# Kernel tuning notes

Hardware: AMD Instinct MI355X
Metric: run time of the kernel (lower is better)

Reference implementation:

```python
import jax, jax.numpy as jnp
import numpy as np

B, S, D = 2, 2048, 2048
H = 16
Q_LORA, KV_LORA = 1536, 512
D_NOPE, D_ROPE = 128, 64
D_QK = D_NOPE + D_ROPE  # 192
D_V = 128
EPS = 1e-6
SCALE = D_QK ** -0.5


def rms_norm(x, w):
    var = jnp.mean(jnp.square(x), axis=-1, keepdims=True)
    return x * jax.lax.rsqrt(var + EPS) * w


def apply_rotary_emb(x, freqs_cis):
    # x: [B, S, h, dr]; freqs_cis: [S, dr//2, 2] (cos, sin); interleaved pairs
    b, s, h, dr = x.shape
    xp = x.reshape(b, s, h, dr // 2, 2)
    x0, x1 = xp[..., 0], xp[..., 1]
    cos = freqs_cis[None, :, None, :, 0]
    sin = freqs_cis[None, :, None, :, 1]
    o0 = x0 * cos - x1 * sin
    o1 = x0 * sin + x1 * cos
    return jnp.stack([o0, o1], axis=-1).reshape(b, s, h, dr)


def setup_inputs() -> dict:
    key = jax.random.key(0)
    ks = jax.random.split(key, 8)
    std = 0.02
    x = jax.random.normal(ks[0], (B, S, D), jnp.float32)
    inv_freq = 1.0 / (10000.0 ** (np.arange(0, D_ROPE, 2, dtype=np.float32) / D_ROPE))
    ang = np.outer(np.arange(S, dtype=np.float32), inv_freq)  # [S, 32]
    freqs_cis = jnp.asarray(np.stack([np.cos(ang), np.sin(ang)], axis=-1))
    return {
        'x': x,
        'freqs_cis': freqs_cis,
        'Wqa': jax.random.normal(ks[1], (Q_LORA, D), jnp.float32) * std,
        'q_a_ln_w': jnp.ones((Q_LORA,), jnp.float32),
        'Wqb': jax.random.normal(ks[2], (H * D_QK, Q_LORA), jnp.float32) * std,
        'Wkva': jax.random.normal(ks[3], (KV_LORA + D_ROPE, D), jnp.float32) * std,
        'kv_a_ln_w': jnp.ones((KV_LORA,), jnp.float32),
        'Wkvb': jax.random.normal(ks[4], (H * (D_NOPE + D_V), KV_LORA), jnp.float32) * std,
        'Wo': jax.random.normal(ks[5], (D, H * D_V), jnp.float32) * std,
    }


def reference(x, freqs_cis, Wqa, q_a_ln_w, Wqb, Wkva, kv_a_ln_w, Wkvb, Wo):
    # Low-rank Q projection: down -> RMSNorm -> up
    q = rms_norm(jnp.einsum('bsd,rd->bsr', x, Wqa), q_a_ln_w)
    q = jnp.einsum('bsr,er->bse', q, Wqb).reshape(B, S, H, D_QK)
    q_nope, q_pe = q[..., :D_NOPE], q[..., D_NOPE:]
    q = jnp.concatenate([q_nope, apply_rotary_emb(q_pe, freqs_cis)], axis=-1)

    # Low-rank KV projection with shared (MQA) rope part
    kv = jnp.einsum('bsd,ed->bse', x, Wkva)
    kv_c, k_pe = kv[..., :KV_LORA], kv[..., KV_LORA:]
    kv_c = rms_norm(kv_c, kv_a_ln_w)
    k_pe = apply_rotary_emb(k_pe[:, :, None, :], freqs_cis)  # [B,S,1,D_ROPE]
    kv = jnp.einsum('bsr,er->bse', kv_c, Wkvb).reshape(B, S, H, D_NOPE + D_V)
    k_nope, v = kv[..., :D_NOPE], kv[..., D_NOPE:]
    k = jnp.concatenate(
        [k_nope, jnp.broadcast_to(k_pe, (B, S, H, D_ROPE))], axis=-1)

    # Causal SDPA with scale = qk_head_dim ** -0.5
    scores = jnp.einsum('bqhd,bkhd->bhqk', q, k) * SCALE
    causal = jnp.tril(jnp.ones((S, S), bool))
    scores = jnp.where(causal[None, None], scores, jnp.finfo(scores.dtype).min)
    probs = jax.nn.softmax(scores, axis=-1)
    out = jnp.einsum('bhqk,bkhd->bqhd', probs, v).reshape(B, S, H * D_V)
    return jnp.einsum('bse,de->bsd', out, Wo)
```

## Files before the change

kernel.cpp:

```cpp
#include <hip/hip_runtime.h>
#include <math.h>

#define B_ 2
#define S_ 2048
#define D_ 2048
#define H_ 16
#define QLORA 1536
#define KVLORA 512
#define DN 128
#define DR 64
#define DQK 192
#define DV 128
#define EPSF 1e-6f
#define SCALEF 0.07216878364870322f

typedef short short8 __attribute__((ext_vector_type(8)));
typedef float float4v __attribute__((ext_vector_type(4)));

__device__ __forceinline__ unsigned short f2bf(float f) {
    union { float f; unsigned u; } x; x.f = f;
    unsigned r = x.u + 0x7fffu + ((x.u >> 16) & 1u);
    return (unsigned short)(r >> 16);
}
__device__ __forceinline__ float bf2f(unsigned short u) {
    union { unsigned u; float f; } x; x.u = (unsigned)u << 16;
    return x.f;
}

#define GLD16(src, dst)                                                        \
    __builtin_amdgcn_global_load_lds(                                          \
        (const __attribute__((address_space(1))) void*)(src),                  \
        (__attribute__((address_space(3))) void*)(dst), 16, 0, 0)

__global__ __launch_bounds__(256) void conv_all(
        const float* __restrict__ s0, unsigned short* __restrict__ d0, long e0,
        const float* __restrict__ s1, unsigned short* __restrict__ d1, long e1,
        const float* __restrict__ s2, unsigned short* __restrict__ d2, long e2,
        const float* __restrict__ s3, unsigned short* __restrict__ d3, long e3,
        const float* __restrict__ s4, unsigned short* __restrict__ d4, long e4,
        const float* __restrict__ s5, unsigned short* __restrict__ d5) {
    long c = (long)blockIdx.x * 256 + threadIdx.x;
    const float* src;
    unsigned short* dst;
    if      (c < e0) { src = s0; dst = d0; }
    else if (c < e1) { src = s1; dst = d1; c -= e0; }
    else if (c < e2) { src = s2; dst = d2; c -= e1; }
    else if (c < e3) { src = s3; dst = d3; c -= e2; }
    else if (c < e4) { src = s4; dst = d4; c -= e3; }
    else             { src = s5; dst = d5; c -= e4; }
    const float* p = src + c * 8;
    float4 a = *(const float4*)(p);
    float4 b = *(const float4*)(p + 4);
    union { short8 v; unsigned short u[8]; } t;
    t.u[0] = f2bf(a.x); t.u[1] = f2bf(a.y); t.u[2] = f2bf(a.z); t.u[3] = f2bf(a.w);
    t.u[4] = f2bf(b.x); t.u[5] = f2bf(b.y); t.u[6] = f2bf(b.z); t.u[7] = f2bf(b.w);
    *(short8*)&dst[c * 8] = t.v;
}

#define GBM 128
#define GBN 128
#define GBK 64

template <typename OT>
__global__ __launch_bounds__(256) void gemm_t(const unsigned short* __restrict__ A,
                                              const unsigned short* __restrict__ W,
                                              OT* __restrict__ C,
                                              int M, int N, int K) {
    __shared__ unsigned short As[GBM * GBK];
    __shared__ unsigned short Ws[GBN * GBK];

    const int tid = threadIdx.x;
    const int w = tid >> 6, lane = tid & 63;
    const int l16 = lane & 15, quad = lane >> 4;
    const int wm = (w >> 1) * 64, wn = (w & 1) * 64;
    const int row0 = blockIdx.y * GBM, col0 = blockIdx.x * GBN;

    const int rL  = lane >> 3;
    const int c8g = (lane & 7) ^ rL;
    const int swzk[2] = { (((0 * 4) + quad) ^ (l16 & 7)) * 8,
                          (((1 * 4) + quad) ^ (l16 & 7)) * 8 };

    const float4v zf = {0.f, 0.f, 0.f, 0.f};
    float4v acc[4][4] = {{zf, zf, zf, zf}, {zf, zf, zf, zf},
                         {zf, zf, zf, zf}, {zf, zf, zf, zf}};

    for (int k0 = 0; k0 < K; k0 += GBK) {
        __syncthreads();
#pragma unroll
        for (int j = 0; j < 4; ++j) {
            const int ch = w * 4 + j;
            const int r = ch * 8 + rL;
            GLD16(&A[(size_t)(row0 + r) * K + k0 + c8g * 8], &As[ch * 512]);
            GLD16(&W[(size_t)(col0 + r) * K + k0 + c8g * 8], &Ws[ch * 512]);
        }
        __syncthreads();

#pragma unroll
        for (int kk = 0; kk < 2; ++kk) {
            const int swz = swzk[kk];
            short8 af[4], bf[4];
#pragma unroll
            for (int mi = 0; mi < 4; ++mi)
                af[mi] = *(const short8*)&As[(wm + mi * 16 + l16) * GBK + swz];
#pragma unroll
            for (int ni = 0; ni < 4; ++ni)
                bf[ni] = *(const short8*)&Ws[(wn + ni * 16 + l16) * GBK + swz];
#pragma unroll
            for (int mi = 0; mi < 4; ++mi)
#pragma unroll
                for (int ni = 0; ni < 4; ++ni)
                    acc[mi][ni] = __builtin_amdgcn_mfma_f32_16x16x32_bf16(af[mi], bf[ni], acc[mi][ni], 0, 0, 0);
        }
    }

#pragma unroll
    for (int mi = 0; mi < 4; ++mi)
#pragma unroll
        for (int ni = 0; ni < 4; ++ni)
#pragma unroll
            for (int r = 0; r < 4; ++r) {
                size_t idx = (size_t)(row0 + wm + mi * 16 + quad * 4 + r) * N + col0 + wn + ni * 16 + l16;
                if constexpr (sizeof(OT) == 2) C[idx] = f2bf(acc[mi][ni][r]);
                else                           C[idx] = acc[mi][ni][r];
            }
}

#define TBM 256
#define TBK 64

template <int MODE, int BN>
__global__ __launch_bounds__(512, 2) void gemm8(const unsigned short* __restrict__ A,
                                                const unsigned short* __restrict__ W,
                                                void* __restrict__ Cp,
                                                unsigned short* __restrict__ Cs,
                                                int M, int N, int K) {
    constexpr int NWCH = BN / 64;
    constexpr int MF = (BN == 256) ? 8 : 4;
    __shared__ unsigned short As[2][TBM * TBK];
    __shared__ unsigned short Ws[2][BN * TBK];

    const int tid = threadIdx.x;
    const int w = tid >> 6, lane = tid & 63;
    const int l16 = lane & 15, quad = lane >> 4;
    const int wm = (BN == 256) ? (w >> 2) * 128 : (w >> 1) * 64;
    const int wn = (BN == 256) ? (w & 3) * 64 : (w & 1) * 64;
    const int row0 = blockIdx.y * TBM, col0 = blockIdx.x * BN;
    const int NT = K / TBK;

    auto stage = [&](int t_, int bufi) {
        const int k0 = t_ * TBK;
#pragma unroll
        for (int i_ = 0; i_ < 4; ++i_) {
            const int ch = i_ * 512 + w * 64 + lane;
            const int r_ = ch >> 3, c_ = ch & 7;
            GLD16(&A[(size_t)(row0 + r_) * K + k0 + ((c_ ^ (r_ & 7)) << 3)],
                  &As[bufi][(i_ * 512 + w * 64) * 8]);
        }
#pragma unroll
        for (int i_ = 0; i_ < NWCH; ++i_) {
            const int ch = i_ * 512 + w * 64 + lane;
            const int r_ = ch >> 3, c_ = ch & 7;
            GLD16(&W[(size_t)(col0 + r_) * K + k0 + ((c_ ^ (r_ & 7)) << 3)],
                  &Ws[bufi][(i_ * 512 + w * 64) * 8]);
        }
    };

    const float4v zf = {0.f, 0.f, 0.f, 0.f};
    float4v acc[MF][4];
#pragma unroll
    for (int mi = 0; mi < MF; ++mi)
#pragma unroll
        for (int ni = 0; ni < 4; ++ni) acc[mi][ni] = zf;

    stage(0, 0);
    stage(1, 1);
    if constexpr (BN == 256) asm volatile("s_waitcnt vmcnt(8)" ::: "memory");
    else                     asm volatile("s_waitcnt vmcnt(6)" ::: "memory");
    __builtin_amdgcn_sched_barrier(0);
    __builtin_amdgcn_s_barrier();
    __builtin_amdgcn_sched_barrier(0);

    for (int t = 0; t < NT; ++t) {
        const int buf = t & 1;
        const unsigned short* Ab = As[buf];
        const unsigned short* Wb = Ws[buf];

        short8 bfr[2][4];
#pragma unroll
        for (int kk = 0; kk < 2; ++kk)
#pragma unroll
            for (int ni = 0; ni < 4; ++ni) {
                const int Rn = wn + ni * 16 + l16;
                bfr[kk][ni] = *(const short8*)&Wb[Rn * TBK + (((kk * 4 + quad) ^ (l16 & 7)) << 3)];
            }
#pragma unroll
        for (int mi = 0; mi < MF; ++mi) {
            const int Rm = wm + mi * 16 + l16;
            short8 a0 = *(const short8*)&Ab[Rm * TBK + (((0 + quad) ^ (l16 & 7)) << 3)];
            short8 a1 = *(const short8*)&Ab[Rm * TBK + (((4 + quad) ^ (l16 & 7)) << 3)];
#pragma unroll
            for (int ni = 0; ni < 4; ++ni) {
                acc[mi][ni] = __builtin_amdgcn_mfma_f32_16x16x32_bf16(a0, bfr[0][ni], acc[mi][ni], 0, 0, 0);
                acc[mi][ni] = __builtin_amdgcn_mfma_f32_16x16x32_bf16(a1, bfr[1][ni], acc[mi][ni], 0, 0, 0);
            }
        }

        __builtin_amdgcn_s_barrier();
        if (t + 2 < NT) {
            stage(t + 2, buf);
            if constexpr (BN == 256) asm volatile("s_waitcnt vmcnt(8)" ::: "memory");
            else                     asm volatile("s_waitcnt vmcnt(6)" ::: "memory");
        } else if (t + 1 < NT) {
            asm volatile("s_waitcnt vmcnt(0)" ::: "memory");
        }
        __builtin_amdgcn_sched_barrier(0);
        __builtin_amdgcn_s_barrier();
        __builtin_amdgcn_sched_barrier(0);
    }

#pragma unroll
    for (int mi = 0; mi < MF; ++mi)
#pragma unroll
        for (int ni = 0; ni < 4; ++ni)
#pragma unroll
            for (int r = 0; r < 4; ++r) {
                const int row = row0 + wm + mi * 16 + quad * 4 + r;
                const int col = col0 + wn + ni * 16 + l16;
                if constexpr (MODE == 0) {
                    ((float*)Cp)[(size_t)row * N + col] = acc[mi][ni][r];
                } else if constexpr (MODE == 1) {
                    ((unsigned short*)Cp)[(size_t)row * N + col] = f2bf(acc[mi][ni][r]);
                } else {
                    const int h = col >> 8, within = col & 255;
                    const unsigned short v = f2bf(acc[mi][ni][r]);
                    if (within < 128) {
                        const int b = row >> 11, s = row & (S_ - 1);
                        Cs[((size_t)(b * H_ + h) * S_ + s) * DQK + within] = v;
                    } else {
                        ((unsigned short*)Cp)[(size_t)row * N + col] = v;
                    }
                }
            }
}

__global__ __launch_bounds__(256) void rmsnorm_b(const float* __restrict__ X,
                                                 const float* __restrict__ w,
                                                 unsigned short* __restrict__ Y,
                                                 int n, int ld) {
    __shared__ float tmp[4];
    const int row = blockIdx.x;
    const int tid = threadIdx.x;
    const float* x = X + (size_t)row * ld;

    float ss = 0.f;
    for (int c = tid; c < n; c += 256) {
        float v = x[c];
        ss = fmaf(v, v, ss);
    }
#pragma unroll
    for (int off = 32; off; off >>= 1) ss += __shfl_xor(ss, off, 64);
    if ((tid & 63) == 0) tmp[tid >> 6] = ss;
    __syncthreads();
    ss = tmp[0] + tmp[1] + tmp[2] + tmp[3];
    float r = rsqrtf(ss / (float)n + EPSF);

    for (int c = tid; c < n; c += 256)
        Y[(size_t)row * n + c] = f2bf(x[c] * r * w[c]);
}

__global__ __launch_bounds__(256) void kv_post(const float* __restrict__ KV,
                                               const float* __restrict__ w,
                                               const float* __restrict__ fc,
                                               unsigned short* __restrict__ kvcb,
                                               unsigned short* __restrict__ Kbf,
                                               int ldkv) {
    __shared__ float tmp[4];
    const int row = blockIdx.x;
    const int s = row & (S_ - 1);
    const int b = row >> 11;
    const int tid = threadIdx.x;
    const float* kv = KV + (size_t)row * ldkv;

    float ss = 0.f;
#pragma unroll
    for (int c = tid; c < KVLORA; c += 256) {
        float v = kv[c];
        ss = fmaf(v, v, ss);
    }
#pragma unroll
    for (int off = 32; off; off >>= 1) ss += __shfl_xor(ss, off, 64);
    if ((tid & 63) == 0) tmp[tid >> 6] = ss;
    __syncthreads();
    ss = tmp[0] + tmp[1] + tmp[2] + tmp[3];
    float r = rsqrtf(ss / (float)KVLORA + EPSF);

#pragma unroll
    for (int c = tid; c < KVLORA; c += 256)
        kvcb[(size_t)row * KVLORA + c] = f2bf(kv[c] * r * w[c]);

    if (tid < 32) {
        int i = tid;
        float c0 = fc[(s * 32 + i) * 2 + 0];
        float s0 = fc[(s * 32 + i) * 2 + 1];
        float x0 = kv[KVLORA + 2 * i];
        float x1 = kv[KVLORA + 2 * i + 1];
        unsigned short b0 = f2bf(x0 * c0 - x1 * s0);
        unsigned short b1 = f2bf(x0 * s0 + x1 * c0);
#pragma unroll
        for (int h = 0; h < H_; ++h) {
            unsigned short* kp = Kbf + ((size_t)(b * H_ + h) * S_ + s) * DQK + DN;
            kp[2 * i]     = b0;
            kp[2 * i + 1] = b1;
        }
    }
}

__global__ __launch_bounds__(256) void pack_vt(const unsigned short* __restrict__ kvbb,
                                               unsigned short* __restrict__ Vt) {
    __shared__ unsigned short T[DV][72];
    const int st = blockIdx.x;
    const int bh = blockIdx.y;
    const int b = bh >> 4, h = bh & 15;
    const int s0 = st * 64;
    const int tid = threadIdx.x;

    for (int c = tid; c < 64 * 16; c += 256) {
        int sp = c >> 4, ch = c & 15;
        short8 v = *(const short8*)&kvbb[(size_t)(b * S_ + s0 + sp) * (H_ * 256) + h * 256 + DN + ch * 8];
        union { short8 v; unsigned short u[8]; } t; t.v = v;
        int dv = ch * 8;
#pragma unroll
        for (int e = 0; e < 8; ++e) T[dv + e][sp] = t.u[e];
    }
    __syncthreads();
    for (int c = tid; c < 128 * 8; c += 256) {
        int dv = c >> 3, ch = c & 7;
        *(short8*)&Vt[((size_t)bh * DV + dv) * S_ + s0 + ch * 8] = *(short8*)&T[dv][ch * 8];
    }
}

#define QTILES 16
#define PROW 76

__global__ __launch_bounds__(512, 1) void flash_mfma(const unsigned short* __restrict__ Qb,
                                                     const float* __restrict__ fc,
                                                     const unsigned short* __restrict__ Kbf,
                                                     const unsigned short* __restrict__ Vt,
                                                     unsigned short* __restrict__ Ob) {
    __shared__ unsigned short Ks[3][64 * 192];
    __shared__ unsigned short Vs[3][128 * 64];
    __shared__ unsigned short Ps[8][16][PROW];

    const int bh = blockIdx.x;
    const int bx = blockIdx.y;
    const int b = bh >> 4, h = bh & 15;
    const int tid = threadIdx.x;
    const int w = tid >> 6, lane = tid & 63;
    const int l16 = lane & 15, quad = lane >> 4;
    const int sw = l16 & 7;

    const unsigned short* Kg = Kbf + (size_t)bh * S_ * DQK;
    const unsigned short* Vg = Vt + (size_t)bh * DV * S_;

    auto stage = [&](int kt_, int bufi) {
        const int kb_ = kt_ * 64;
#pragma unroll
        for (int i_ = 0; i_ < 3; ++i_) {
            int ch = (w * 3 + i_) * 64 + lane;
            int r_ = ch / 24, c_ = ch - r_ * 24;
            GLD16(&Kg[(size_t)(kb_ + r_) * DQK + ((c_ ^ (r_ & 7)) << 3)],
                  &Ks[bufi][(w * 3 + i_) * 512]);
        }
#pragma unroll
        for (int i_ = 0; i_ < 2; ++i_) {
            int ch = (w * 2 + i_) * 64 + lane;
            int r_ = ch >> 3, c_ = ch & 7;
            GLD16(&Vg[(size_t)r_ * S_ + kb_ + ((c_ ^ (r_ & 7)) << 3)],
                  &Vs[bufi][(w * 2 + i_) * 512]);
        }
    };

    for (int half = 0; half < 2; ++half) {
        const int qt = half ? (QTILES - 1 - bx) : bx;
        const int q0 = qt * 128;
        const int ntiles = 2 * qt + 2;
        const int wr0 = q0 + w * 16;

        short8 a_q[6];
        {
            const int s = wr0 + l16;
            const unsigned short* qrow = Qb + (size_t)(b * S_ + s) * (H_ * DQK) + h * DQK;
#pragma unroll
            for (int i = 0; i < 6; ++i) {
                short8 t = *(const short8*)&qrow[i * 32 + quad * 8];
                if (i >= 4) {
                    union { short8 v; unsigned short u[8]; } x; x.v = t;
#pragma unroll
                    for (int j = 0; j < 4; ++j) {
                        int ip = (i - 4) * 16 + quad * 4 + j;
                        float c0 = fc[(s * 32 + ip) * 2 + 0];
                        float s0 = fc[(s * 32 + ip) * 2 + 1];
                        float x0 = bf2f(x.u[2 * j]);
                        float x1 = bf2f(x.u[2 * j + 1]);
                        x.u[2 * j]     = f2bf(x0 * c0 - x1 * s0);
                        x.u[2 * j + 1] = f2bf(x0 * s0 + x1 * c0);
                    }
                    t = x.v;
                }
                a_q[i] = t;
            }
        }

        stage(0, 0);
        if (ntiles > 1) stage(1, 1);
        asm volatile("s_waitcnt vmcnt(5)" ::: "memory");
        __builtin_amdgcn_sched_barrier(0);
        __builtin_amdgcn_s_barrier();
        __builtin_amdgcn_sched_barrier(0);

        const float4v zf = {0.f, 0.f, 0.f, 0.f};
        float4v o_acc[8] = {zf, zf, zf, zf, zf, zf, zf, zf};
        float l_r[4] = {0.f, 0.f, 0.f, 0.f};

        int cb = 0;
        for (int kt = 0; kt < ntiles; ++kt) {
            const int kb = kt * 64;

            if (kt + 2 < ntiles) {
                int sb = cb + 2; if (sb >= 3) sb -= 3;
                stage(kt + 2, sb);
            }

            if (kb <= wr0 + 15) {
                const unsigned short* Kb_ = Ks[cb];
                const unsigned short* Vb_ = Vs[cb];

                float4v sc[4] = {zf, zf, zf, zf};
#pragma unroll
                for (int i = 0; i < 6; ++i) {
                    short8 bk[4];
#pragma unroll
                    for (int kg = 0; kg < 4; ++kg)
                        bk[kg] = *(const short8*)&Kb_[(kg * 16 + l16) * 192 + (((i * 4 + quad) ^ sw) << 3)];
#pragma unroll
                    for (int kg = 0; kg < 4; ++kg)
                        sc[kg] = __builtin_amdgcn_mfma_f32_16x16x32_bf16(a_q[i], bk[kg], sc[kg], 0, 0, 0);
                }

                const bool mneed = (kb + 63 > wr0);
#pragma unroll
                for (int kg = 0; kg < 4; ++kg) {
                    const int key = kb + kg * 16 + l16;
#pragma unroll
                    for (int r = 0; r < 4; ++r) {
                        float p = __expf(sc[kg][r] * SCALEF);
                        if (mneed && key > wr0 + quad * 4 + r) p = 0.f;
                        l_r[r] += p;
                        Ps[w][quad * 4 + r][kg * 16 + l16] = f2bf(p);
                    }
                }

#pragma unroll
                for (int kc = 0; kc < 2; ++kc) {
                    short8 pa = *(const short8*)&Ps[w][l16][kc * 32 + quad * 8];
#pragma unroll
                    for (int dvt = 0; dvt < 8; ++dvt) {
                        short8 vb = *(const short8*)&Vb_[(dvt * 16 + l16) * 64 + (((kc * 4 + quad) ^ sw) << 3)];
                        o_acc[dvt] = __builtin_amdgcn_mfma_f32_16x16x32_bf16(pa, vb, o_acc[dvt], 0, 0, 0);
                    }
                }
            }

            if (kt + 2 < ntiles) {
                asm volatile("s_waitcnt vmcnt(5)" ::: "memory");
            } else if (kt + 1 < ntiles) {
                asm volatile("s_waitcnt vmcnt(0)" ::: "memory");
            }
            __builtin_amdgcn_sched_barrier(0);
            __builtin_amdgcn_s_barrier();
            __builtin_amdgcn_sched_barrier(0);

            cb = (cb == 2) ? 0 : cb + 1;
        }

#pragma unroll
        for (int r = 0; r < 4; ++r) {
            float t = l_r[r];
            t += __shfl_xor(t, 1);
            t += __shfl_xor(t, 2);
            t += __shfl_xor(t, 4);
            t += __shfl_xor(t, 8);
            l_r[r] = t;
        }
#pragma unroll
        for (int r = 0; r < 4; ++r) {
            float inv = 1.f / l_r[r];
            int row = wr0 + quad * 4 + r;
            unsigned short* op = Ob + (size_t)(b * S_ + row) * (H_ * DV) + h * DV;
#pragma unroll
            for (int dvt = 0; dvt < 8; ++dvt)
                op[dvt * 16 + l16] = f2bf(o_acc[dvt][r] * inv);
        }
    }
}

extern "C" void kernel_launch(void* const* d_in, const int* in_sizes, int n_in,
                              void* d_out, int out_size, void* d_ws, size_t ws_size,
                              hipStream_t stream) {
    const float* x    = (const float*)d_in[0];
    const float* fc   = (const float*)d_in[1];
    const float* Wqa  = (const float*)d_in[2];
    const float* qlw  = (const float*)d_in[3];
    const float* Wqb  = (const float*)d_in[4];
    const float* Wkva = (const float*)d_in[5];
    const float* kvw  = (const float*)d_in[6];
    const float* Wkvb = (const float*)d_in[7];
    const float* Wo   = (const float*)d_in[8];
    float* out = (float*)d_out;

    const int M = B_ * S_;
    const int NQKV = QLORA + 640;
    char* wsb = (char*)d_ws;

    unsigned short* qb  = (unsigned short*)wsb;
    unsigned short* Wob = (unsigned short*)(wsb + 25165824);
    char* R2 = wsb + 50331648;
    float*          qlkv  = (float*)R2;
    unsigned short* xb    = (unsigned short*)(R2 + 35651584);
    unsigned short* Wcat  = (unsigned short*)(R2 + 52428800);
    unsigned short* kvbb  = (unsigned short*)R2;
    unsigned short* attnb = (unsigned short*)R2;
    char* R3 = R2 + 67108864;
    unsigned short* qlatb = (unsigned short*)R3;
    unsigned short* Wqbb  = (unsigned short*)(R3 + 12582912);
    unsigned short* Kbf   = (unsigned short*)R3;
    char* R4 = R3 + 25165824;
    unsigned short* kvcb  = (unsigned short*)(R4 + 1048576);
    unsigned short* Wkvbb = (unsigned short*)(R4 + 5242880);
    unsigned short* Vt    = (unsigned short*)R4;

    {
        const long e0 = 1048576;
        const long e1 = e0 + 393216;
        const long e2 = e1 + 147456;
        const long e3 = e2 + 589824;
        const long e4 = e3 + 262144;
        const long tot = e4 + 524288;
        conv_all<<<(int)(tot / 256), 256, 0, stream>>>(
            x, xb, e0,
            Wqa, Wcat, e1,
            Wkva, Wcat + (size_t)QLORA * D_, e2,
            Wqb, Wqbb, e3,
            Wkvb, Wkvbb, e4,
            Wo, Wob);
    }

    gemm_t<float><<<dim3(NQKV / GBN, M / GBM), 256, 0, stream>>>(xb, Wcat, qlkv, M, NQKV, D_);

    rmsnorm_b<<<M, 256, 0, stream>>>(qlkv, qlw, qlatb, QLORA, NQKV);

    gemm8<1, 256><<<dim3(H_ * DQK / 256, M / TBM), 512, 0, stream>>>(qlatb, Wqbb, qb, nullptr, M, H_ * DQK, QLORA);

    kv_post<<<M, 256, 0, stream>>>(qlkv + QLORA, kvw, fc, kvcb, Kbf, NQKV);

    gemm8<2, 256><<<dim3(H_ * 256 / 256, M / TBM), 512, 0, stream>>>(kvcb, Wkvbb, kvbb, Kbf, M, H_ * 256, KVLORA);

    pack_vt<<<dim3(S_ / 64, B_ * H_), 256, 0, stream>>>(kvbb, Vt);

    flash_mfma<<<dim3(B_ * H_, QTILES / 2), 512, 0, stream>>>(qb, fc, Kbf, Vt, attnb);

    gemm8<0, 128><<<dim3(D_ / 128, M / TBM), 512, 0, stream>>>(attnb, Wob, out, nullptr, M, D_, D_);
}
```

Measured before the change: 436.9 us.

## Fuse V transpose into KV up-projection epilogue and reuse gemm8 for down-projection

The KV up-projection GEMM epilogue now transposes the V half through a swizzled shared-memory tile and writes Vt directly. This removes the separate pack_vt kernel and the kvbb intermediate round trip through global memory. The first fused Q/KV down-projection also switches from the simpler gemm_t kernel to the double-buffered 256x128 gemm8 kernel. NQKV=2176 is divisible by 128, so the tiling fits. The epilogue adds an extra __syncthreads and reuses the As buffer as scratch.

```diff
diff --git a/kernel.cpp b/kernel.cpp
--- a/kernel.cpp
+++ b/kernel.cpp
@@ -57,74 +57,6 @@
     *(short8*)&dst[c * 8] = t.v;
 }
 
-#define GBM 128
-#define GBN 128
-#define GBK 64
-
-template <typename OT>
-__global__ __launch_bounds__(256) void gemm_t(const unsigned short* __restrict__ A,
-                                              const unsigned short* __restrict__ W,
-                                              OT* __restrict__ C,
-                                              int M, int N, int K) {
-    __shared__ unsigned short As[GBM * GBK];
-    __shared__ unsigned short Ws[GBN * GBK];
-
-    const int tid = threadIdx.x;
-    const int w = tid >> 6, lane = tid & 63;
-    const int l16 = lane & 15, quad = lane >> 4;
-    const int wm = (w >> 1) * 64, wn = (w & 1) * 64;
-    const int row0 = blockIdx.y * GBM, col0 = blockIdx.x * GBN;
-
-    const int rL  = lane >> 3;
-    const int c8g = (lane & 7) ^ rL;
-    const int swzk[2] = { (((0 * 4) + quad) ^ (l16 & 7)) * 8,
-                          (((1 * 4) + quad) ^ (l16 & 7)) * 8 };
-
-    const float4v zf = {0.f, 0.f, 0.f, 0.f};
-    float4v acc[4][4] = {{zf, zf, zf, zf}, {zf, zf, zf, zf},
-                         {zf, zf, zf, zf}, {zf, zf, zf, zf}};
-
-    for (int k0 = 0; k0 < K; k0 += GBK) {
-        __syncthreads();
-#pragma unroll
-        for (int j = 0; j < 4; ++j) {
-            const int ch = w * 4 + j;
-            const int r = ch * 8 + rL;
-            GLD16(&A[(size_t)(row0 + r) * K + k0 + c8g * 8], &As[ch * 512]);
-            GLD16(&W[(size_t)(col0 + r) * K + k0 + c8g * 8], &Ws[ch * 512]);
-        }
-        __syncthreads();
-
-#pragma unroll
-        for (int kk = 0; kk < 2; ++kk) {
-            const int swz = swzk[kk];
-            short8 af[4], bf[4];
-#pragma unroll
-            for (int mi = 0; mi < 4; ++mi)
-                af[mi] = *(const short8*)&As[(wm + mi * 16 + l16) * GBK + swz];
-#pragma unroll
-            for (int ni = 0; ni < 4; ++ni)
-                bf[ni] = *(const short8*)&Ws[(wn + ni * 16 + l16) * GBK + swz];
-#pragma unroll
-            for (int mi = 0; mi < 4; ++mi)
-#pragma unroll
-                for (int ni = 0; ni < 4; ++ni)
-                    acc[mi][ni] = __builtin_amdgcn_mfma_f32_16x16x32_bf16(af[mi], bf[ni], acc[mi][ni], 0, 0, 0);
-        }
-    }
-
-#pragma unroll
-    for (int mi = 0; mi < 4; ++mi)
-#pragma unroll
-        for (int ni = 0; ni < 4; ++ni)
-#pragma unroll
-            for (int r = 0; r < 4; ++r) {
-                size_t idx = (size_t)(row0 + wm + mi * 16 + quad * 4 + r) * N + col0 + wn + ni * 16 + l16;
-                if constexpr (sizeof(OT) == 2) C[idx] = f2bf(acc[mi][ni][r]);
-                else                           C[idx] = acc[mi][ni][r];
-            }
-}
-
 #define TBM 256
 #define TBK 64
 
@@ -218,29 +150,60 @@
         __builtin_amdgcn_sched_barrier(0);
     }
 
-#pragma unroll
-    for (int mi = 0; mi < MF; ++mi)
-#pragma unroll
-        for (int ni = 0; ni < 4; ++ni)
-#pragma unroll
-            for (int r = 0; r < 4; ++r) {
-                const int row = row0 + wm + mi * 16 + quad * 4 + r;
-                const int col = col0 + wn + ni * 16 + l16;
-                if constexpr (MODE == 0) {
-                    ((float*)Cp)[(size_t)row * N + col] = acc[mi][ni][r];
-                } else if constexpr (MODE == 1) {
-                    ((unsigned short*)Cp)[(size_t)row * N + col] = f2bf(acc[mi][ni][r]);
-                } else {
-                    const int h = col >> 8, within = col & 255;
-                    const unsigned short v = f2bf(acc[mi][ni][r]);
-                    if (within < 128) {
-                        const int b = row >> 11, s = row & (S_ - 1);
-                        Cs[((size_t)(b * H_ + h) * S_ + s) * DQK + within] = v;
-                    } else {
-                        ((unsigned short*)Cp)[(size_t)row * N + col] = v;
+    if constexpr (MODE != 2) {
+#pragma unroll
+        for (int mi = 0; mi < MF; ++mi)
+#pragma unroll
+            for (int ni = 0; ni < 4; ++ni)
+#pragma unroll
+                for (int r = 0; r < 4; ++r) {
+                    const int row = row0 + wm + mi * 16 + quad * 4 + r;
+                    const int col = col0 + wn + ni * 16 + l16;
+                    if constexpr (MODE == 0)
+                        ((float*)Cp)[(size_t)row * N + col] = acc[mi][ni][r];
+                    else
+                        ((unsigned short*)Cp)[(size_t)row * N + col] = f2bf(acc[mi][ni][r]);
+                }
+    } else {
+        const int h = blockIdx.x;
+        const int b = row0 >> 11, s0 = row0 & (S_ - 1);
+        char* Tb = (char*)&As[0][0];
+        if (wn < 128) {
+#pragma unroll
+            for (int mi = 0; mi < MF; ++mi)
+#pragma unroll
+                for (int ni = 0; ni < 4; ++ni)
+#pragma unroll
+                    for (int r = 0; r < 4; ++r) {
+                        const int sl = wm + mi * 16 + quad * 4 + r;
+                        const int d = wn + ni * 16 + l16;
+                        Cs[((size_t)(b * H_ + h) * S_ + s0 + sl) * DQK + d] = f2bf(acc[mi][ni][r]);
                     }
+        } else {
+#pragma unroll
+            for (int mi = 0; mi < MF; ++mi)
+#pragma unroll
+                for (int ni = 0; ni < 4; ++ni) {
+                    const int dv = wn - 128 + ni * 16 + l16;
+                    const int sl = wm + mi * 16 + quad * 4;
+                    union { unsigned short u[4]; uint2 v; } pk;
+                    pk.u[0] = f2bf(acc[mi][ni][0]);
+                    pk.u[1] = f2bf(acc[mi][ni][1]);
+                    pk.u[2] = f2bf(acc[mi][ni][2]);
+                    pk.u[3] = f2bf(acc[mi][ni][3]);
+                    *(uint2*)(Tb + dv * 512 + ((sl * 2) ^ ((dv & 7) << 4))) = pk.v;
                 }
-            }
+        }
+        __syncthreads();
+        unsigned short* VtP = (unsigned short*)Cp;
+#pragma unroll
+        for (int i = 0; i < 8; ++i) {
+            const int idx = i * 512 + tid;
+            const int dv = idx >> 5, sc = idx & 31;
+            short8 v = *(const short8*)(Tb + dv * 512 + ((sc * 16) ^ ((dv & 7) << 4)));
+            *(short8*)&VtP[((size_t)((b * H_ + h) * DV + dv)) * S_ + s0 + sc * 8] = v;
+        }
+    }
 }
 
 __global__ __launch_bounds__(256) void rmsnorm_b(const float* __restrict__ X,
@@ -312,30 +275,6 @@
             kp[2 * i]     = b0;
             kp[2 * i + 1] = b1;
         }
-    }
-}
-
-__global__ __launch_bounds__(256) void pack_vt(const unsigned short* __restrict__ kvbb,
-                                               unsigned short* __restrict__ Vt) {
-    __shared__ unsigned short T[DV][72];
-    const int st = blockIdx.x;
-    const int bh = blockIdx.y;
-    const int b = bh >> 4, h = bh & 15;
-    const int s0 = st * 64;
-    const int tid = threadIdx.x;
-
-    for (int c = tid; c < 64 * 16; c += 256) {
-        int sp = c >> 4, ch = c & 15;
-        short8 v = *(const short8*)&kvbb[(size_t)(b * S_ + s0 + sp) * (H_ * 256) + h * 256 + DN + ch * 8];
-        union { short8 v; unsigned short u[8]; } t; t.v = v;
-        int dv = ch * 8;
-#pragma unroll
-        for (int e = 0; e < 8; ++e) T[dv + e][sp] = t.u[e];
-    }
-    __syncthreads();
-    for (int c = tid; c < 128 * 8; c += 256) {
-        int dv = c >> 3, ch = c & 7;
-        *(short8*)&Vt[((size_t)bh * DV + dv) * S_ + s0 + ch * 8] = *(short8*)&T[dv][ch * 8];
     }
 }
 
@@ -528,8 +467,8 @@
     float*          qlkv  = (float*)R2;
     unsigned short* xb    = (unsigned short*)(R2 + 35651584);
     unsigned short* Wcat  = (unsigned short*)(R2 + 52428800);
-    unsigned short* kvbb  = (unsigned short*)R2;
     unsigned short* attnb = (unsigned short*)R2;
+    unsigned short* Vt    = (unsigned short*)(R2 + 16777216);
     char* R3 = R2 + 67108864;
     unsigned short* qlatb = (unsigned short*)R3;
     unsigned short* Wqbb  = (unsigned short*)(R3 + 12582912);
@@ -537,7 +476,6 @@
     char* R4 = R3 + 25165824;
     unsigned short* kvcb  = (unsigned short*)(R4 + 1048576);
     unsigned short* Wkvbb = (unsigned short*)(R4 + 5242880);
-    unsigned short* Vt    = (unsigned short*)R4;
 
     {
         const long e0 = 1048576;
@@ -555,7 +493,7 @@
             Wo, Wob);
     }
 
-    gemm_t<float><<<dim3(NQKV / GBN, M / GBM), 256, 0, stream>>>(xb, Wcat, qlkv, M, NQKV, D_);
+    gemm8<0, 128><<<dim3(NQKV / 128, M / TBM), 512, 0, stream>>>(xb, Wcat, qlkv, nullptr, M, NQKV, D_);
 
     rmsnorm_b<<<M, 256, 0, stream>>>(qlkv, qlw, qlatb, QLORA, NQKV);
 
@@ -563,9 +501,7 @@
 
     kv_post<<<M, 256, 0, stream>>>(qlkv + QLORA, kvw, fc, kvcb, Kbf, NQKV);
 
-    gemm8<2, 256><<<dim3(H_ * 256 / 256, M / TBM), 512, 0, stream>>>(kvcb, Wkvbb, kvbb, Kbf, M, H_ * 256, KVLORA);
-
-    pack_vt<<<dim3(S_ / 64, B_ * H_), 256, 0, stream>>>(kvbb, Vt);
+    gemm8<2, 256><<<dim3(H_ * 256 / 256, M / TBM), 512, 0, stream>>>(kvcb, Wkvbb, Vt, Kbf, M, H_ * 256, KVLORA);
 
     flash_mfma<<<dim3(B_ * H_, QTILES / 2), 512, 0, stream>>>(qb, fc, Kbf, Vt, attnb);
 
```

Result: no change. 430.0 us (-1.6%).
